# Kernel optimization log

Hardware: AMD Instinct MI355X
Metric: run time of the kernel (lower is better)

The kernel has to match this reference:

```python
import jax, jax.numpy as jnp
import numpy as np


def setup_inputs() -> dict:
    key = jax.random.key(0)
    k1, k2, k3, k4 = jax.random.split(key, 4)
    N, C, H, W = 1, 512, 192, 192
    F, K = 512, 3
    x = jax.random.normal(k1, (N, C, H, W), dtype=jnp.float32)
    w = jax.random.normal(k2, (F, C, K, K), dtype=jnp.float32) * 0.05
    b = jax.random.normal(k3, (F,), dtype=jnp.float32)
    # binary RoI mask over output spatial grid (stands in for PIL polygon raster)
    mask = jax.random.randint(k4, (H, W), 0, 2, dtype=jnp.int32)
    return {"x": x, "w": w, "b": b, "mask": mask}


def reference(x, w, b, mask):
    # my_conv: im2col conv (stride=1, pad=1), gather rows where mask==1,
    # GEMM, scatter back into zeros, then add bias everywhere (res += b
    # happens AFTER the scatter). Equivalent dense form: conv(x,w)*mask + b.
    conv = jax.lax.conv_general_dilated(
        x, w,
        window_strides=(1, 1),
        padding=((1, 1), (1, 1)),
        dimension_numbers=("NCHW", "OIHW", "NCHW"),
    )  # [N, F, H, W]
    m = mask.astype(conv.dtype)[None, None, :, :]
    return conv * m + b[None, :, None, None]
```

## Files before the change

### kernel.cpp

```cpp
#include <hip/hip_runtime.h>


typedef unsigned short ushort_t;
typedef __attribute__((ext_vector_type(8))) __bf16 bf16x8;
typedef __attribute__((ext_vector_type(4))) float f32x4;
typedef __attribute__((ext_vector_type(8))) unsigned short ushort8;

#define IMG_W 192
#define IMG_H 192
#define HW    36864
#define PAD_W 194
#define C_IN  512
#define F_OUT 512
#define KTOT  4608
#define NCBLK 144

__device__ __forceinline__ unsigned short f2bf(float f) {
  unsigned int u = __builtin_bit_cast(unsigned int, f);
  u += 0x7fffu + ((u >> 16) & 1u);
  return (unsigned short)(u >> 16);
}

__device__ __forceinline__ void async16(const void* g, void* l) {
  __builtin_amdgcn_global_load_lds(
      (const __attribute__((address_space(1))) unsigned int*)g,
      (__attribute__((address_space(3))) unsigned int*)l, 16, 0, 0);
}

__global__ void mega_prep(const float* __restrict__ x, const float* __restrict__ w,
                          const float* __restrict__ bias, const int* __restrict__ mask,
                          ushort_t* __restrict__ Xt, ushort_t* __restrict__ Wt,
                          int* __restrict__ list, int* __restrict__ counter,
                          float* __restrict__ out) {
  __shared__ float tile[64][65];
  __shared__ int red[4], wpc[4], woff[4];
  const int bid = blockIdx.x;
  const int tid = threadIdx.x;

  if (bid < 4608) {
    const int p  = bid;
    const int w0 = (p % 3) * 64;
    const int c0 = ((p / 3) & 7) * 64;
    const int h  = p / 24;

    const int wl_r = tid & 63;
    const int cg_r = tid >> 6;
    const float* src = x + (size_t)(c0 + cg_r * 16) * HW + (size_t)h * IMG_W + w0 + wl_r;
#pragma unroll
    for (int cc = 0; cc < 16; ++cc)
      tile[cg_r * 16 + cc][wl_r] = src[(size_t)cc * HW];
    __syncthreads();

    const int wl = tid >> 2;
    const int cg = tid & 3;
    ushort_t* dst = Xt + ((size_t)(h + 1) * PAD_W + (w0 + wl + 1)) * C_IN + c0 + cg * 16;
    ushort8 v0, v1;
#pragma unroll
    for (int cc = 0; cc < 8; ++cc) v0[cc] = f2bf(tile[cg * 16 + cc][wl]);
#pragma unroll
    for (int cc = 0; cc < 8; ++cc) v1[cc] = f2bf(tile[cg * 16 + 8 + cc][wl]);
    *(ushort8*)dst = v0;
    *(ushort8*)(dst + 8) = v1;
  } else if (bid < 4801) {
    const int idx = (bid - 4608) * 256 + tid;
    const int p   = idx >> 6;
    const int off = (idx & 63) * 8;
    int r, c;
    if (p < 388) { r = (p >= 194) ? 193 : 0; c = (p >= 194) ? p - 194 : p; }
    else         { int q = p - 388; r = 1 + (q >> 1); c = (q & 1) ? 193 : 0; }
    ushort8 z = {0, 0, 0, 0, 0, 0, 0, 0};
    *(ushort8*)(Xt + ((size_t)r * PAD_W + c) * C_IN + off) = z;
  } else if (bid < 5825) {
    const int idx = (bid - 4801) * 256 + tid;
    const int f = idx >> 9;
    const int c = idx & 511;
    const float* src = w + (size_t)idx * 9;
    float v[9];
#pragma unroll
    for (int t = 0; t < 9; ++t) v[t] = src[t];
    ushort_t* dst = Wt + (size_t)f * KTOT + c;
#pragma unroll
    for (int t = 0; t < 9; ++t) dst[t * C_IN] = f2bf(v[t]);
  } else if (bid < 5969) {
    const int cbid = bid - 5825;
    const int lane = tid & 63;
    const int wave = tid >> 6;
    const int i = cbid * 256 + tid;
    const int m = mask[i];
    unsigned long long b = __ballot(m != 0);
    int pcnt = 0;
    for (int k = tid; k < cbid * 256; k += 256) pcnt += (mask[k] != 0) ? 1 : 0;
#pragma unroll
    for (int off = 32; off; off >>= 1) pcnt += __shfl_down(pcnt, off);
    if (lane == 0) { red[wave] = pcnt; wpc[wave] = __popcll(b); }
    __syncthreads();
    if (tid == 0) {
      const int acc = red[0] + red[1] + red[2] + red[3];
      woff[0] = acc;
      woff[1] = acc + wpc[0];
      woff[2] = acc + wpc[0] + wpc[1];
      woff[3] = acc + wpc[0] + wpc[1] + wpc[2];
      if (cbid == NCBLK - 1)
        counter[0] = acc + wpc[0] + wpc[1] + wpc[2] + wpc[3];
    }
    __syncthreads();
    if (m) list[woff[wave] + __popcll(b & ((1ull << lane) - 1ull))] = i;
  } else {
    const int g = (bid - 5969) * 256 + tid;
    f32x4* o4 = (f32x4*)out;
#pragma unroll
    for (int it = 0; it < 9; ++it) {
      const int n4 = g + it * 524288;
      const int f  = n4 / (HW / 4);
      const float bv = bias[f];
      f32x4 v = {bv, bv, bv, bv};
      o4[n4] = v;
    }
  }
}

__global__ __launch_bounds__(256, 3) void conv_gemm(
    const ushort_t* __restrict__ Wt, const ushort_t* __restrict__ Xt,
    const float* __restrict__ bias, const int* __restrict__ list,
    const int* __restrict__ counter, float* __restrict__ out) {
  __shared__ __align__(16) ushort_t As[128 * 64];
  __shared__ __align__(16) ushort_t Bs[128 * 64];

  const int count = counter[0];
  const int n0 = blockIdx.x * 128;
  if (n0 >= count) return;

  const int tid  = threadIdx.x;
  const int lane = tid & 63;
  const int wave = tid >> 6;
  const int wm   = wave >> 1;
  const int wn   = wave & 1;
  const int m0   = blockIdx.y * 128;

  const int rrel = lane >> 3;
  const int q    = (lane & 7) ^ rrel;

  const ushort_t* aSrc = Wt + (size_t)(m0 + wave * 32 + rrel) * KTOT + q * 8;

  unsigned int bOffs[4];
#pragma unroll
  for (int ii = 0; ii < 4; ++ii) {
    const int pos = n0 + wave * 32 + ii * 8 + rrel;
    const int pix = (pos < count) ? list[pos] : 0;
    const int hh = pix / IMG_W, ww = pix - hh * IMG_W;
    bOffs[ii] = ((hh + 1) * PAD_W + (ww + 1)) * C_IN + q * 8;
  }

  ushort_t* aDst = &As[wave * 32 * 64];
  ushort_t* bDst = &Bs[wave * 32 * 64];

  const int col  = lane & 15;
  const int quad = lane >> 4;

  f32x4 acc[4][4] = {};

  {
    const int toff0 = -(PAD_W + 1) * C_IN;
#pragma unroll
    for (int ii = 0; ii < 4; ++ii) {
      async16(aSrc + (size_t)ii * 8 * KTOT, aDst + ii * 512);
      async16(Xt + (int)bOffs[ii] + toff0, bDst + ii * 512);
    }
  }

#pragma unroll 1
  for (int kk = 0; kk < 72; ++kk) {
    __syncthreads();
    bf16x8 af[2][4], bfr[2][4];
#pragma unroll
    for (int s = 0; s < 2; ++s) {
#pragma unroll
      for (int i = 0; i < 4; ++i) {
        const int row = wm * 64 + i * 16 + col;
        af[s][i] = *(const bf16x8*)&As[row * 64 + ((s * 4 + quad) ^ (row & 7)) * 8];
      }
#pragma unroll
      for (int j = 0; j < 4; ++j) {
        const int row = wn * 64 + j * 16 + col;
        bfr[s][j] = *(const bf16x8*)&Bs[row * 64 + ((s * 4 + quad) ^ (row & 7)) * 8];
      }
    }
    if (kk < 71) {
      __syncthreads();
      const int kn   = kk + 1;
      const int tapn = kn >> 3;
      const int kcn  = (kn & 7) * 64;
      const int toffn = ((tapn / 3) * PAD_W + (tapn % 3) - (PAD_W + 1)) * C_IN;
      const int aoffn = tapn * 512 + kcn;
#pragma unroll
      for (int ii = 0; ii < 4; ++ii) {
        async16(aSrc + (size_t)ii * 8 * KTOT + aoffn, aDst + ii * 512);
        async16(Xt + (int)bOffs[ii] + toffn + kcn, bDst + ii * 512);
      }
    }
#pragma unroll
    for (int s = 0; s < 2; ++s)
#pragma unroll
      for (int i = 0; i < 4; ++i)
#pragma unroll
        for (int j = 0; j < 4; ++j)
          acc[i][j] = __builtin_amdgcn_mfma_f32_16x16x32_bf16(af[s][i], bfr[s][j],
                                                              acc[i][j], 0, 0, 0);
  }

#pragma unroll
  for (int j = 0; j < 4; ++j) {
    const int pos = n0 + wn * 64 + j * 16 + col;
    if (pos < count) {
      const int n_pix = list[pos];
#pragma unroll
      for (int i = 0; i < 4; ++i) {
        const int mrow = m0 + wm * 64 + i * 16 + quad * 4;
        float* o = out + (size_t)mrow * HW + n_pix;
#pragma unroll
        for (int r = 0; r < 4; ++r)
          o[(size_t)r * HW] = acc[i][j][r] + bias[mrow + r];
      }
    }
  }
}

extern "C" void kernel_launch(void* const* d_in, const int* in_sizes, int n_in,
                              void* d_out, int out_size, void* d_ws, size_t ws_size,
                              hipStream_t stream) {
  const float* x    = (const float*)d_in[0];
  const float* w    = (const float*)d_in[1];
  const float* bias = (const float*)d_in[2];
  const int*   mask = (const int*)d_in[3];
  float* out = (float*)d_out;

  int* list    = (int*)d_ws;
  int* counter = list + HW;
  ushort_t* Xt = (ushort_t*)((char*)d_ws + 148096);
  ushort_t* Wt = Xt + (size_t)PAD_W * PAD_W * C_IN;

  mega_prep<<<dim3(8017), 256, 0, stream>>>(x, w, bias, mask, Xt, Wt, list,
                                            counter, out);
  conv_gemm<<<dim3((HW + 127) / 128, F_OUT / 128), 256, 0, stream>>>(
      Wt, Xt, bias, list, counter, out);
}
```

Measured before the change: 266.7 us.

## Fuse bias fill into GEMM epilogue with coalesced dense row writes

Drops the separate bias-broadcast pass over the whole output in the prep kernel. Each GEMM block now owns the pixel range covered by its slice of the sorted mask list and writes that range densely: masked pixels get accumulator plus bias, unmasked ones get bias alone. Accumulators are staged through LDS and matched to pixels through a slot table, so rows are written with coalesced stores instead of scattered per-pixel stores. This avoids writing the output twice, at the cost of extra LDS traffic, barriers and an epilogue that loops over pixel chunks.

Result: slower. 294.6 us (+10.4%).

```diff
diff --git a/kernel.cpp b/kernel.cpp
--- a/kernel.cpp
+++ b/kernel.cpp
@@ -14,6 +14,7 @@
 #define F_OUT 512
 #define KTOT  4608
 #define NCBLK 144
+#define EPI_CHUNK 1024
 
 __device__ __forceinline__ unsigned short f2bf(float f) {
   unsigned int u = __builtin_bit_cast(unsigned int, f);
@@ -28,10 +29,9 @@
 }
 
 __global__ void mega_prep(const float* __restrict__ x, const float* __restrict__ w,
-                          const float* __restrict__ bias, const int* __restrict__ mask,
+                          const int* __restrict__ mask,
                           ushort_t* __restrict__ Xt, ushort_t* __restrict__ Wt,
-                          int* __restrict__ list, int* __restrict__ counter,
-                          float* __restrict__ out) {
+                          int* __restrict__ list, int* __restrict__ counter) {
   __shared__ float tile[64][65];
   __shared__ int red[4], wpc[4], woff[4];
   const int bid = blockIdx.x;
@@ -81,7 +81,7 @@
     ushort_t* dst = Wt + (size_t)f * KTOT + c;
 #pragma unroll
     for (int t = 0; t < 9; ++t) dst[t * C_IN] = f2bf(v[t]);
-  } else if (bid < 5969) {
+  } else {
     const int cbid = bid - 5825;
     const int lane = tid & 63;
     const int wave = tid >> 6;
@@ -105,17 +105,6 @@
     }
     __syncthreads();
     if (m) list[woff[wave] + __popcll(b & ((1ull << lane) - 1ull))] = i;
-  } else {
-    const int g = (bid - 5969) * 256 + tid;
-    f32x4* o4 = (f32x4*)out;
-#pragma unroll
-    for (int it = 0; it < 9; ++it) {
-      const int n4 = g + it * 524288;
-      const int f  = n4 / (HW / 4);
-      const float bv = bias[f];
-      f32x4 v = {bv, bv, bv, bv};
-      o4[n4] = v;
-    }
   }
 }
 
@@ -125,17 +114,37 @@
     const int* __restrict__ counter, float* __restrict__ out) {
   __shared__ __align__(16) ushort_t As[128 * 64];
   __shared__ __align__(16) ushort_t Bs[128 * 64];
+  float* sm  = (float*)As;
+  int* slot  = (int*)((char*)Bs + 1024);
 
   const int count = counter[0];
   const int n0 = blockIdx.x * 128;
-  if (n0 >= count) return;
-
+  const int m0 = blockIdx.y * 128;
   const int tid  = threadIdx.x;
+
+  int lo_pix, hi_pix;
+  {
+    const int loPos = n0, hiPos = n0 + 128;
+    lo_pix = (loPos == 0) ? 0 : ((loPos <= count) ? list[loPos - 1] + 1 : HW);
+    hi_pix = (hiPos <= count) ? list[hiPos - 1] + 1 : HW;
+    if (hi_pix < lo_pix) hi_pix = lo_pix;
+  }
+
+  if (n0 >= count) {
+    for (int rr = 0; rr < 128; ++rr) {
+      const float bv = bias[m0 + rr];
+      float* o = out + (size_t)(m0 + rr) * HW;
+      for (int p = lo_pix + tid; p < hi_pix; p += 256) o[p] = bv;
+    }
+    return;
+  }
+
   const int lane = tid & 63;
   const int wave = tid >> 6;
   const int wm   = wave >> 1;
   const int wn   = wave & 1;
-  const int m0   = blockIdx.y * 128;
+
+  const int mypix = (tid < 128 && n0 + tid < count) ? list[n0 + tid] : -1;
 
   const int rrel = lane >> 3;
   const int q    = (lane & 7) ^ rrel;
@@ -208,20 +217,37 @@
                                                               acc[i][j], 0, 0, 0);
   }
 
-#pragma unroll
-  for (int j = 0; j < 4; ++j) {
-    const int pos = n0 + wn * 64 + j * 16 + col;
-    if (pos < count) {
-      const int n_pix = list[pos];
-#pragma unroll
-      for (int i = 0; i < 4; ++i) {
-        const int mrow = m0 + wm * 64 + i * 16 + quad * 4;
-        float* o = out + (size_t)mrow * HW + n_pix;
-#pragma unroll
-        for (int r = 0; r < 4; ++r)
-          o[(size_t)r * HW] = acc[i][j][r] + bias[mrow + r];
-      }
-    }
+  __syncthreads();
+#pragma unroll
+  for (int i = 0; i < 4; ++i) {
+#pragma unroll
+    for (int j = 0; j < 4; ++j)
+#pragma unroll
+      for (int r = 0; r < 4; ++r)
+        sm[(wm * 16 + quad * 4 + r) * 132 + wn * 64 + j * 16 + col] = acc[i][j][r];
+    __syncthreads();
+#pragma unroll 1
+    for (int c0 = lo_pix; c0 < hi_pix; c0 += EPI_CHUNK) {
+      const int c1 = (c0 + EPI_CHUNK < hi_pix) ? c0 + EPI_CHUNK : hi_pix;
+#pragma unroll
+      for (int t = 0; t < EPI_CHUNK / 256; ++t) slot[t * 256 + tid] = -1;
+      __syncthreads();
+      if (mypix >= c0 && mypix < c1) slot[mypix - c0] = tid;
+      __syncthreads();
+#pragma unroll 1
+      for (int rI = 0; rI < 32; ++rI) {
+        const int mrow = m0 + (rI >> 4) * 64 + i * 16 + (rI & 15);
+        const float bv = bias[mrow];
+        const float* smr = sm + rI * 132;
+        float* o = out + (size_t)mrow * HW;
+        for (int p = c0 + tid; p < c1; p += 256) {
+          const int s = slot[p - c0];
+          o[p] = (s >= 0) ? smr[s] + bv : bv;
+        }
+      }
+      __syncthreads();
+    }
+    __syncthreads();
   }
 }
 
@@ -239,8 +265,7 @@
   ushort_t* Xt = (ushort_t*)((char*)d_ws + 148096);
   ushort_t* Wt = Xt + (size_t)PAD_W * PAD_W * C_IN;
 
-  mega_prep<<<dim3(8017), 256, 0, stream>>>(x, w, bias, mask, Xt, Wt, list,
-                                            counter, out);
+  mega_prep<<<dim3(5969), 256, 0, stream>>>(x, w, mask, Xt, Wt, list, counter);
   conv_gemm<<<dim3((HW + 127) / 128, F_OUT / 128), 256, 0, stream>>>(
       Wt, Xt, bias, list, counter, out);
 }
```

## Add L3 prefetch kernel and XCD-aware block remapping for conv GEMM

Applied to the files above, without the earlier changes.

Adds a kernel that reads x and w before the prep kernel, trying to warm the last-level cache so the transpose and convert work hits in cache. The GEMM grid is flattened to 1D and the active block IDs are remapped so consecutive tiles land on the same XCD: each tile's four M blocks sharing an N range run on one XCD, which aims to improve L2 reuse of the gathered Xt rows. The prefetch adds a full extra pass over the inputs (about 75 MB for x plus w), which may cost more than it saves.

New measurement: 287.8 us. +7.9%, slower.

```diff
diff --git a/kernel.cpp b/kernel.cpp
--- a/kernel.cpp
+++ b/kernel.cpp
@@ -25,6 +25,24 @@
   __builtin_amdgcn_global_load_lds(
       (const __attribute__((address_space(1))) unsigned int*)g,
       (__attribute__((address_space(3))) unsigned int*)l, 16, 0, 0);
+}
+
+__global__ void prefetch_l3(const float* __restrict__ x,
+                            const float* __restrict__ w) {
+  const int g = blockIdx.x * 256 + threadIdx.x;
+  const f32x4* x4 = (const f32x4*)x;
+  float s = 0.f;
+#pragma unroll
+  for (int it = 0; it < 9; ++it) {
+    f32x4 v = x4[g + it * 524288];
+    s += v[0];
+  }
+  const f32x4* w4 = (const f32x4*)w;
+  for (int idx = g; idx < 589824; idx += 524288) {
+    f32x4 v = w4[idx];
+    s += v[0];
+  }
+  asm volatile("" :: "v"(s));
 }
 
 __global__ void mega_prep(const float* __restrict__ x, const float* __restrict__ w,
@@ -127,15 +145,21 @@
   __shared__ __align__(16) ushort_t Bs[128 * 64];
 
   const int count = counter[0];
-  const int n0 = blockIdx.x * 128;
-  if (n0 >= count) return;
+  const int nact   = (count + 127) >> 7;
+  const int active = nact * 4;
+  const int orig   = blockIdx.x;
+  if (orig >= active) return;
+  const int qq = active >> 3, rr8 = active & 7;
+  const int xcd = orig & 7, sfr = orig >> 3;
+  const int wgid = (xcd < rr8 ? xcd * (qq + 1) : rr8 * (qq + 1) + (xcd - rr8) * qq) + sfr;
+  const int n0 = (wgid >> 2) * 128;
+  const int m0 = (wgid & 3) * 128;
 
   const int tid  = threadIdx.x;
   const int lane = tid & 63;
   const int wave = tid >> 6;
   const int wm   = wave >> 1;
   const int wn   = wave & 1;
-  const int m0   = blockIdx.y * 128;
 
   const int rrel = lane >> 3;
   const int q    = (lane & 7) ^ rrel;
@@ -239,8 +263,8 @@
   ushort_t* Xt = (ushort_t*)((char*)d_ws + 148096);
   ushort_t* Wt = Xt + (size_t)PAD_W * PAD_W * C_IN;
 
+  prefetch_l3<<<dim3(2048), 256, 0, stream>>>(x, w);
   mega_prep<<<dim3(8017), 256, 0, stream>>>(x, w, bias, mask, Xt, Wt, list,
                                             counter, out);
-  conv_gemm<<<dim3((HW + 127) / 128, F_OUT / 128), 256, 0, stream>>>(
-      Wt, Xt, bias, list, counter, out);
-}
+  conv_gemm<<<dim3(288 * 4), 256, 0, stream>>>(Wt, Xt, bias, list, counter, out);
+}
```
